# Performance work log

Measured on AMD Instinct MI355X. Metric: run time of the kernel, lower is better.

## Reference

```python
import jax, jax.numpy as jnp
import numpy as np

B, H, W, C = 2, 64, 64, 96
DIN, NST, RNK, K = 192, 16, 6, 4
L = H * W


def _make_ids():
    idx = np.arange(L).reshape(H, W)
    p0 = idx.reshape(-1)
    p1 = idx.T.reshape(-1)
    p2 = p0[::-1].copy()
    p3 = p1[::-1].copy()
    scan = np.stack([p0, p1, p2, p3]).astype(np.int32)
    inv = np.stack([np.argsort(p) for p in scan]).astype(np.int32)
    return jnp.asarray(scan), jnp.asarray(inv)


def setup_inputs() -> dict:
    key = jax.random.key(0)
    ks = jax.random.split(key, 10)
    scan_ids, inv_ids = _make_ids()
    std = RNK ** -0.5
    # dt bias init: inverse-softplus of dt ~ LogUniform(1e-3, 1e-1), as in VMM.dt_init
    u = jax.random.uniform(ks[5], (K, DIN))
    dt = jnp.exp(u * (np.log(0.1) - np.log(0.001)) + np.log(0.001))
    dt_b = dt + jnp.log(-jnp.expm1(-dt))
    return {
        "x": jax.random.normal(ks[0], (B, H, W, C), jnp.float32),
        "W_in": jax.random.normal(ks[1], (2 * DIN, C), jnp.float32) * 0.02,
        "conv_w": jax.random.normal(ks[2], (DIN, 1, 3, 3), jnp.float32) * 0.1,
        "conv_b": jnp.zeros((DIN,), jnp.float32),
        "x_proj_w": jax.random.normal(ks[3], (K, RNK + 2 * NST, DIN), jnp.float32) * 0.02,
        "dt_w": jax.random.uniform(ks[4], (K, DIN, RNK), jnp.float32, -std, std),
        "dt_b": dt_b.astype(jnp.float32),
        "A_logs": jnp.log(jnp.tile(jnp.arange(1, NST + 1, dtype=jnp.float32)[None], (K * DIN, 1))),
        "Ds": jnp.ones((K * DIN,), jnp.float32),
        "gate_w": jax.random.normal(ks[6], (4 * DIN, 4), jnp.float32) * 0.1,  # grouped 1x1 conv, groups=DIN
        "gate_b": jnp.zeros((4 * DIN,), jnp.float32),
        "ln_g": jnp.ones((DIN,), jnp.float32),
        "ln_b": jnp.zeros((DIN,), jnp.float32),
        "W_out": jax.random.normal(ks[7], (C, DIN), jnp.float32) * 0.02,
        "scan_ids": scan_ids,
        "inv_ids": inv_ids,
    }


def _forward(x, W_in, conv_w, conv_b, x_proj_w, dt_w, dt_b, A_logs, Ds, gate_w, gate_b, ln_g, ln_b, W_out, scan_ids, inv_ids):
    b, h, w, c = x.shape
    l = h * w
    din = conv_w.shape[0]
    k = x_proj_w.shape[0]
    nst = A_logs.shape[1]
    rnk = dt_w.shape[2]
    # in_proj + split into x / gate z
    xz = x @ W_in.T
    xc, z = jnp.split(xz, 2, axis=-1)
    xc = jnp.transpose(xc, (0, 3, 1, 2))  # (b, din, h, w)
    # depthwise 3x3 conv + SiLU
    xc = jax.lax.conv_general_dilated(
        xc, conv_w, (1, 1), "SAME", feature_group_count=din,
        dimension_numbers=("NCHW", "OIHW", "NCHW")) + conv_b[None, :, None, None]
    xc = jax.nn.silu(xc)
    # multi-directional gather (mair_ids_scan)
    xf = xc.reshape(b, din, l)
    xs = jnp.moveaxis(xf[:, :, scan_ids], 2, 1)  # (b, k, din, l)
    # x_proj (grouped 1x1 conv) -> dt, B, C
    x_dbl = jnp.einsum("bkdl,krd->bkrl", xs, x_proj_w)
    dts, Bs, Cs = jnp.split(x_dbl, [rnk, rnk + nst], axis=2)  # (b,k,rnk,l),(b,k,n,l),(b,k,n,l)
    delta = jax.nn.softplus(jnp.einsum("bkrl,kdr->bkdl", dts, dt_w) + dt_b[None, :, :, None])
    A = -jnp.exp(A_logs).reshape(k, din, nst)
    dA = jnp.exp(delta[..., None] * A[None, :, :, None, :])              # (b,k,d,l,n)
    dBu = (delta * xs)[..., None] * jnp.moveaxis(Bs, 2, 3)[:, :, None]   # (b,k,d,l,n)

    def step(hst, inp):
        da, dbu = inp
        hst = da * hst + dbu
        return hst, hst

    h0 = jnp.zeros((b, k, din, nst), jnp.float32)
    _, hs = jax.lax.scan(step, h0, (jnp.moveaxis(dA, 3, 0), jnp.moveaxis(dBu, 3, 0)))  # (l,b,k,d,n)
    ys = jnp.einsum("lbkdn,bknl->bkdl", hs, Cs) + xs * Ds.reshape(k, din)[None, :, :, None]
    # inverse scatter (mair_ids_inverse) + concat along channels
    y = jax.vmap(lambda yk, ik: yk[..., ik], in_axes=(1, 0), out_axes=1)(ys, inv_ids)
    y = y.reshape(b, k * din, h, w)
    # ShuffleAttn gating: group = din, group_channels = k
    shuf = y.reshape(b, k, din, h, w).transpose(0, 2, 1, 3, 4).reshape(b, k * din, h, w)
    pooled = shuf.mean(axis=(2, 3)).reshape(b, din, k)
    gate = jax.nn.sigmoid(jnp.einsum("bgi,goi->bgo", pooled, gate_w.reshape(din, k, k)) + gate_b.reshape(din, k))
    gate = gate.transpose(0, 2, 1).reshape(b, k * din)  # channel_rearrange
    y = y * gate[:, :, None, None]
    # sum the 4 direction branches
    y = y.reshape(b, k, din, h, w).sum(axis=1)
    y = jnp.transpose(y, (0, 2, 3, 1))  # (b,h,w,din)
    # LayerNorm(d_inner)
    mu = y.mean(-1, keepdims=True)
    var = ((y - mu) ** 2).mean(-1, keepdims=True)
    y = (y - mu) / jnp.sqrt(var + 1e-5) * ln_g + ln_b
    y = y * jax.nn.silu(z)
    return y @ W_out.T


def reference(x, W_in, conv_w, conv_b, x_proj_w, dt_w, dt_b, A_logs, Ds, gate_w, gate_b, ln_g, ln_b, W_out, scan_ids, inv_ids):
    return _forward(x, W_in, conv_w, conv_b, x_proj_w, dt_w, dt_b, A_logs, Ds, gate_w, gate_b, ln_g, ln_b, W_out, scan_ids, inv_ids)
```

## Files before the change

### kernel.cpp

```cpp
#include <hip/hip_runtime.h>
#include <math.h>

#define BB 2
#define CC 96
#define DIN 192
#define NST 16
#define RNK 6
#define KK 4
#define LL 4096
#define RTOT (RNK + 2*NST)


__global__ __launch_bounds__(256) void k_inproj(const float* __restrict__ x,
        const float* __restrict__ W_in, float* __restrict__ xc_pre,
        float* __restrict__ z_silu) {
    __shared__ float lx[96*65];
    __shared__ float wt[48*196];
    int b = blockIdx.y, z = blockIdx.z;
    int l0 = blockIdx.x * 64;
    int t = threadIdx.x;
    for (int i = 0; i < 24; ++i) {
        int e = t + 256*i;
        int l = e / 96, c = e % 96;
        lx[c*65 + l] = x[((size_t)(b*LL + l0 + l))*96 + c];
    }
    int lg = t & 15;
    int og = t >> 4;
    float acc[4][12];
    #pragma unroll
    for (int j = 0; j < 4; ++j)
        #pragma unroll
        for (int q = 0; q < 12; ++q) acc[j][q] = 0.f;
    for (int p = 0; p < 2; ++p) {
        __syncthreads();
        for (int i = 0; i < 36; ++i) {
            int e = t + 256*i;
            int cc = e % 48, oc = e / 48;
            wt[cc*196 + oc] = W_in[((size_t)(z*192 + oc))*96 + p*48 + cc];
        }
        __syncthreads();
        #pragma unroll 2
        for (int cc = 0; cc < 48; ++cc) {
            int c = p*48 + cc;
            float x0 = lx[c*65 + 4*lg + 0];
            float x1 = lx[c*65 + 4*lg + 1];
            float x2 = lx[c*65 + 4*lg + 2];
            float x3 = lx[c*65 + 4*lg + 3];
            const float* wr = &wt[cc*196 + 12*og];
            float4 w0 = *(const float4*)(wr);
            float4 w1 = *(const float4*)(wr + 4);
            float4 w2 = *(const float4*)(wr + 8);
            float wv[12] = {w0.x,w0.y,w0.z,w0.w, w1.x,w1.y,w1.z,w1.w,
                            w2.x,w2.y,w2.z,w2.w};
            #pragma unroll
            for (int q = 0; q < 12; ++q) {
                acc[0][q] += x0*wv[q];
                acc[1][q] += x1*wv[q];
                acc[2][q] += x2*wv[q];
                acc[3][q] += x3*wv[q];
            }
        }
    }
    float* dst = (z == 0) ? xc_pre : z_silu;
    #pragma unroll
    for (int j = 0; j < 4; ++j) {
        int l = l0 + 4*lg + j;
        size_t base = (size_t)(b*LL + l)*DIN + 12*og;
        #pragma unroll
        for (int q = 0; q < 12; ++q) {
            float v = acc[j][q];
            if (z) v = v / (1.f + __expf(-v));
            dst[base + q] = v;
        }
    }
}

__global__ __launch_bounds__(256) void k_conv(const float* __restrict__ xc,
        const float* __restrict__ cw, const float* __restrict__ cb,
        float* __restrict__ out) {
    int gid = blockIdx.x*256 + threadIdx.x;
    int d = gid % DIN;
    int r = gid / DIN;
    int l = r & 4095, b = r >> 12;
    int w = l & 63, h = l >> 6;
    float acc = cb[d];
    #pragma unroll
    for (int dh = -1; dh <= 1; ++dh) {
        int h2 = h + dh;
        bool okh = (h2 >= 0) && (h2 < 64);
        #pragma unroll
        for (int dw = -1; dw <= 1; ++dw) {
            int w2 = w + dw;
            if (okh && w2 >= 0 && w2 < 64)
                acc += xc[((size_t)(b*LL + h2*64 + w2))*DIN + d] * cw[d*9 + (dh+1)*3 + (dw+1)];
        }
    }
    out[((size_t)(b*LL + l))*DIN + d] = acc / (1.f + __expf(-acc));
}

__global__ __launch_bounds__(512) void k_proj(const float* __restrict__ xconv,
        const int* __restrict__ scan_ids, const float* __restrict__ xpw,
        float* __restrict__ dts, float* __restrict__ Bs, float* __restrict__ Cs) {
    __shared__ float lxs[96*65];
    __shared__ float lw[RTOT*96];
    __shared__ float lbc[64*33];
    __shared__ int lsid[64];
    int k = blockIdx.y, b = blockIdx.z;
    int l0 = blockIdx.x * 64;
    int t = threadIdx.x;
    if (t < 64) lsid[t] = scan_ids[k*LL + l0 + t];
    int l = t & 63;
    int rg = __builtin_amdgcn_readfirstlane(t >> 6);
    float acc[5];
    #pragma unroll
    for (int j = 0; j < 5; ++j) acc[j] = 0.f;
    for (int p = 0; p < 2; ++p) {
        __syncthreads();
        for (int i = 0; i < 12; ++i) {
            int e = t + 512*i;
            int dd = e % 96, ll = e / 96;
            lxs[dd*65 + ll] = xconv[((size_t)(b*LL + lsid[ll]))*DIN + p*96 + dd];
        }
        for (int i = 0; i < 8; ++i) {
            int e = t + 512*i;
            if (e < RTOT*96) {
                int r = e / 96, dd = e % 96;
                lw[r*96 + dd] = xpw[(size_t)k*RTOT*DIN + r*DIN + p*96 + dd];
            }
        }
        __syncthreads();
        for (int dd = 0; dd < 96; dd += 4) {
            float x0 = lxs[(dd+0)*65 + l];
            float x1 = lxs[(dd+1)*65 + l];
            float x2 = lxs[(dd+2)*65 + l];
            float x3 = lxs[(dd+3)*65 + l];
            #pragma unroll
            for (int j = 0; j < 5; ++j) {
                int r = rg + 8*j;
                if (r < RTOT) {
                    float4 w = *(const float4*)&lw[r*96 + dd];
                    acc[j] += x0*w.x + x1*w.y + x2*w.z + x3*w.w;
                }
            }
        }
    }
    int bk = b*KK + k;
    #pragma unroll
    for (int j = 0; j < 5; ++j) {
        int r = rg + 8*j;
        if (r < RNK)       dts[((size_t)bk*LL + l0 + l)*8 + r] = acc[j];
        else if (r < RTOT) lbc[l*33 + (r - RNK)] = acc[j];
    }
    __syncthreads();
    size_t rowb = ((size_t)bk*LL + l0)*NST;
    for (int i = 0; i < 2; ++i) {
        int e = t + 512*i;
        int n = e & 15, ll = e >> 4;
        Bs[rowb + ll*NST + n] = lbc[ll*33 + n];
        Cs[rowb + ll*NST + n] = lbc[ll*33 + 16 + n];
    }
}

__global__ __launch_bounds__(384) void k_scan1(const float* __restrict__ xconv,
        const float* __restrict__ Bs, const float* __restrict__ Cs,
        const float* __restrict__ dts, const float* __restrict__ dtw,
        const float* __restrict__ dtb,
        const int* __restrict__ scan_ids, const float* __restrict__ A_logs,
        const float* __restrict__ Ds,
        float* __restrict__ y_dirs, float* __restrict__ segA,
        float* __restrict__ segB, int SL) {
    int seg = blockIdx.x, bk = blockIdx.y;
    int b = bk >> 2, k = bk & 3;
    int t = threadIdx.x;
    int half = t & 1, d = t >> 1;
    int l0 = seg * SL;
    float Av[8];
    {
        const float4* ap = (const float4*)(A_logs + ((k*DIN + d)*NST + half*8));
        float4 a0 = ap[0], a1 = ap[1];
        Av[0]=-__expf(a0.x); Av[1]=-__expf(a0.y); Av[2]=-__expf(a0.z); Av[3]=-__expf(a0.w);
        Av[4]=-__expf(a1.x); Av[5]=-__expf(a1.y); Av[6]=-__expf(a1.z); Av[7]=-__expf(a1.w);
    }
    float Dv = Ds[k*DIN + d];
    float wdt[RNK];
    float bdt = dtb[k*DIN + d];
    #pragma unroll
    for (int r = 0; r < RNK; ++r) wdt[r] = dtw[(k*DIN + d)*RNK + r];
    float h[8];
    #pragma unroll
    for (int n = 0; n < 8; ++n) h[n] = 0.f;
    float sumdv = 0.f;
    const int* sid = scan_ids + k*LL + l0;
    int ln = sid[0];
    float xn = xconv[((size_t)(b*LL + ln))*DIN + d];
    for (int li = 0; li < SL; ++li) {
        int l = ln;
        float xv = xn;
        if (li + 1 < SL) {
            ln = sid[li + 1];
            xn = xconv[((size_t)(b*LL + ln))*DIN + d];
        }
        const float* dr = dts + ((size_t)bk*LL + l0 + li)*8;
        float aa = bdt;
        #pragma unroll
        for (int r = 0; r < RNK; ++r) aa += dr[r]*wdt[r];
        float dv = fmaxf(aa, 0.f) + __logf(1.f + __expf(-fabsf(aa)));
        sumdv += dv;
        float dxv = dv * xv;
        const float* br = Bs + ((size_t)bk*LL + l0 + li)*NST + half*8;
        const float* cr = Cs + ((size_t)bk*LL + l0 + li)*NST + half*8;
        float4 b0 = *(const float4*)br;
        float4 b1 = *(const float4*)(br + 4);
        float4 c0v = *(const float4*)cr;
        float4 c1v = *(const float4*)(cr + 4);
        float bb[8] = {b0.x,b0.y,b0.z,b0.w, b1.x,b1.y,b1.z,b1.w};
        float cc[8] = {c0v.x,c0v.y,c0v.z,c0v.w, c1v.x,c1v.y,c1v.z,c1v.w};
        float y = 0.f;
        #pragma unroll
        for (int n = 0; n < 8; ++n) {
            float e2 = __expf(dv * Av[n]);
            h[n] = e2*h[n] + dxv*bb[n];
            y += h[n]*cc[n];
        }
        y += __shfl_xor(y, 1);
        if (half == 0) {
            y += xv * Dv;
            y_dirs[((size_t)(bk*LL + l))*DIN + d] = y;
        }
    }
    float a[8];
    #pragma unroll
    for (int n = 0; n < 8; ++n) a[n] = __expf(Av[n]*sumdv);
    size_t base = (((size_t)bk*gridDim.x + seg)*DIN + d)*NST + half*8;
    *(float4*)&segA[base]     = make_float4(a[0],a[1],a[2],a[3]);
    *(float4*)&segA[base + 4] = make_float4(a[4],a[5],a[6],a[7]);
    *(float4*)&segB[base]     = make_float4(h[0],h[1],h[2],h[3]);
    *(float4*)&segB[base + 4] = make_float4(h[4],h[5],h[6],h[7]);
}

__global__ __launch_bounds__(256) void k_scan2(const float* segA,
        const float* segB, float* hinit, int SEGC) {
    int idx = blockIdx.x*256 + threadIdx.x;
    if (idx >= BB*KK*DIN*NST) return;
    int bk = idx / (DIN*NST);
    int dn = idx % (DIN*NST);
    const size_t stride = DIN*NST;
    size_t o = (size_t)bk*SEGC*stride + dn;
    float h = 0.f;
    for (int s = 0; s < SEGC; s += 8) {
        float av[8], bv[8];
        #pragma unroll
        for (int j = 0; j < 8; ++j) {
            av[j] = segA[o + j*stride];
            bv[j] = segB[o + j*stride];
        }
        #pragma unroll
        for (int j = 0; j < 8; ++j) {
            hinit[o + j*stride] = h;
            h = av[j]*h + bv[j];
        }
        o += 8*stride;
    }
}

__global__ __launch_bounds__(384) void k_apply(const float* __restrict__ Cs,
        const float* __restrict__ dts, const float* __restrict__ dtw,
        const float* __restrict__ dtb,
        const int* __restrict__ scan_ids, const float* __restrict__ A_logs,
        const float* __restrict__ hinit,
        float* __restrict__ y_dirs, float* __restrict__ poolsum, int SL) {
    int seg = blockIdx.x, bk = blockIdx.y;
    int b = bk >> 2, k = bk & 3;
    int t = threadIdx.x;
    int half = t & 1, d = t >> 1;
    int l0 = seg * SL;
    float Av[8];
    {
        const float4* ap = (const float4*)(A_logs + ((k*DIN + d)*NST + half*8));
        float4 a0 = ap[0], a1 = ap[1];
        Av[0]=-__expf(a0.x); Av[1]=-__expf(a0.y); Av[2]=-__expf(a0.z); Av[3]=-__expf(a0.w);
        Av[4]=-__expf(a1.x); Av[5]=-__expf(a1.y); Av[6]=-__expf(a1.z); Av[7]=-__expf(a1.w);
    }
    float Av0 = -__expf(A_logs[(k*DIN + d)*NST]);
    bool okl = true;
    #pragma unroll
    for (int q = 0; q < 8; ++q) {
        float m = (float)(half*8 + q + 1);
        okl = okl && (fabsf(Av[q] - m*Av0) <= 1e-4f*m);
    }
    int fast = __all(okl);
    float h0[8];
    {
        size_t base = (((size_t)bk*gridDim.x + seg)*DIN + d)*NST + half*8;
        float4 v0 = *(const float4*)&hinit[base];
        float4 v1 = *(const float4*)&hinit[base + 4];
        h0[0]=v0.x; h0[1]=v0.y; h0[2]=v0.z; h0[3]=v0.w;
        h0[4]=v1.x; h0[5]=v1.y; h0[6]=v1.z; h0[7]=v1.w;
    }
    float wdt[RNK];
    float bdt = dtb[k*DIN + d];
    #pragma unroll
    for (int r = 0; r < RNK; ++r) wdt[r] = dtw[(k*DIN + d)*RNK + r];
    float cum = 0.f;
    float pool = 0.f;
    const int* sid = scan_ids + k*LL + l0;
    for (int li = 0; li < SL; ++li) {
        int l = sid[li];
        const float* dr = dts + ((size_t)bk*LL + l0 + li)*8;
        float aa = bdt;
        #pragma unroll
        for (int r = 0; r < RNK; ++r) aa += dr[r]*wdt[r];
        cum += fmaxf(aa, 0.f) + __logf(1.f + __expf(-fabsf(aa)));
        const float* cr = Cs + ((size_t)bk*LL + l0 + li)*NST + half*8;
        float4 c0v = *(const float4*)cr;
        float4 c1v = *(const float4*)(cr + 4);
        float cc[8] = {c0v.x,c0v.y,c0v.z,c0v.w, c1v.x,c1v.y,c1v.z,c1v.w};
        float g;
        if (fast) {
            float E = __expf(Av0 * cum);
            g = 0.f;
            #pragma unroll
            for (int q = 7; q >= 0; --q) g = g*E + cc[q]*h0[q];
            g *= E;
            if (half) {
                float E2 = E*E, E4 = E2*E2;
                g *= E4*E4;
            }
        } else {
            g = 0.f;
            #pragma unroll
            for (int q = 0; q < 8; ++q)
                g += cc[q]*h0[q]*__expf(Av[q]*cum);
        }
        g += __shfl_xor(g, 1);
        if (half == 0) {
            size_t yo = ((size_t)(bk*LL + l))*DIN + d;
            float y = y_dirs[yo] + g;
            y_dirs[yo] = y;
            pool += y;
        }
    }
    if (half == 0) atomicAdd(&poolsum[(b*DIN + d)*KK + k], pool);
}

__global__ __launch_bounds__(256) void k_final(const float* __restrict__ y_dirs,
        const float* __restrict__ poolsum, const float* __restrict__ gw,
        const float* __restrict__ gb, const float* __restrict__ z_silu,
        const float* __restrict__ lng, const float* __restrict__ lnb,
        const float* __restrict__ Wout, float* __restrict__ out) {
    __shared__ float buf[16*193];
    __shared__ float lgate[DIN*KK];
    __shared__ float lmu[16], lrs[16];
    int b = blockIdx.y;
    int l0 = blockIdx.x * 16;
    int t = threadIdx.x;
    for (int e = t; e < DIN*KK; e += 256) {
        int d = e >> 2, o = e & 3;
        float acc = gb[d*KK + o];
        #pragma unroll
        for (int i = 0; i < KK; ++i)
            acc += (poolsum[(b*DIN + d)*KK + i] * (1.f/LL)) * gw[(d*KK + o)*KK + i];
        lgate[d*KK + o] = 1.f/(1.f + __expf(-acc));
    }
    __syncthreads();
    for (int i = 0; i < 12; ++i) {
        int e = t + 256*i;
        int d = e % DIN, l = e / DIN;
        float acc = 0.f;
        #pragma unroll
        for (int k = 0; k < KK; ++k)
            acc += y_dirs[((size_t)((b*KK + k)*LL + l0 + l))*DIN + d] * lgate[d*KK + k];
        buf[l*193 + d] = acc;
    }
    __syncthreads();
    int l2 = t >> 4, q = t & 15;
    float s = 0.f, s2 = 0.f;
    for (int i = 0; i < 12; ++i) {
        float v = buf[l2*193 + q + 16*i];
        s += v; s2 += v*v;
    }
    s += __shfl_xor(s, 1);  s2 += __shfl_xor(s2, 1);
    s += __shfl_xor(s, 2);  s2 += __shfl_xor(s2, 2);
    s += __shfl_xor(s, 4);  s2 += __shfl_xor(s2, 4);
    s += __shfl_xor(s, 8);  s2 += __shfl_xor(s2, 8);
    if (q == 0) {
        float mu = s * (1.f/DIN);
        float var = s2 * (1.f/DIN) - mu*mu;
        lmu[l2] = mu;
        lrs[l2] = rsqrtf(var + 1e-5f);
    }
    __syncthreads();
    for (int i = 0; i < 12; ++i) {
        int e = t + 256*i;
        int d = e % DIN, l = e / DIN;
        float v = buf[l*193 + d];
        float tv = (v - lmu[l]) * lrs[l] * lng[d] + lnb[d];
        tv *= z_silu[((size_t)(b*LL + l0 + l))*DIN + d];
        buf[l*193 + d] = tv;
    }
    __syncthreads();
    int l = t & 15;
    int c0 = (t >> 4) * 6;
    float acc[6];
    #pragma unroll
    for (int cc = 0; cc < 6; ++cc) acc[cc] = 0.f;
    for (int d = 0; d < DIN; ++d) {
        float v = buf[l*193 + d];
        #pragma unroll
        for (int cc = 0; cc < 6; ++cc)
            acc[cc] += v * Wout[(c0 + cc)*DIN + d];
    }
    #pragma unroll
    for (int cc = 0; cc < 6; ++cc)
        out[((size_t)(b*LL + l0 + l))*CC + c0 + cc] = acc[cc];
}

extern "C" void kernel_launch(void* const* d_in, const int* in_sizes, int n_in,
                              void* d_out, int out_size, void* d_ws, size_t ws_size,
                              hipStream_t stream) {
    const float* x      = (const float*)d_in[0];
    const float* W_in   = (const float*)d_in[1];
    const float* conv_w = (const float*)d_in[2];
    const float* conv_b = (const float*)d_in[3];
    const float* xpw    = (const float*)d_in[4];
    const float* dt_w   = (const float*)d_in[5];
    const float* dt_b   = (const float*)d_in[6];
    const float* A_logs = (const float*)d_in[7];
    const float* Ds     = (const float*)d_in[8];
    const float* gate_w = (const float*)d_in[9];
    const float* gate_b = (const float*)d_in[10];
    const float* ln_g   = (const float*)d_in[11];
    const float* ln_b   = (const float*)d_in[12];
    const float* W_out  = (const float*)d_in[13];
    const int* scan_ids = (const int*)d_in[14];
    float* out = (float*)d_out;

    const size_t baseF = 6291456ull + 2ull*1572864 + 262144ull + 2ull*524288 + 3072;
    int SEGC = 16;
    if ((baseF + 2ull*128*24576)*4 <= ws_size) SEGC = 128;
    else if ((baseF + 2ull*64*24576)*4 <= ws_size) SEGC = 64;
    else if ((baseF + 2ull*32*24576)*4 <= ws_size) SEGC = 32;
    int SL = LL / SEGC;
    size_t segF = (size_t)SEGC * 24576;

    float* ws      = (float*)d_ws;
    float* y_dirs  = ws;
    float* xc_pre  = ws;
    float* z_silu  = y_dirs  + 6291456;
    float* xconv   = z_silu  + 1572864;
    float* dts     = xconv   + 1572864;
    float* Bs      = dts     + 262144;
    float* Cs      = Bs      + 524288;
    float* poolsum = Cs      + 524288;
    float* segA    = poolsum + 3072;
    float* segB    = segA    + segF;
    float* hinit   = segA;

    hipMemsetAsync(poolsum, 0, 1536*sizeof(float), stream);

    k_inproj<<<dim3(LL/64, BB, 2), 256, 0, stream>>>(x, W_in, xc_pre, z_silu);
    k_conv<<<(BB*DIN*LL)/256, 256, 0, stream>>>(xc_pre, conv_w, conv_b, xconv);
    k_proj<<<dim3(LL/64, KK, BB), 512, 0, stream>>>(xconv, scan_ids, xpw,
                                                    dts, Bs, Cs);
    k_scan1<<<dim3(SEGC, BB*KK), 384, 0, stream>>>(xconv, Bs, Cs, dts, dt_w, dt_b,
                                                   scan_ids, A_logs, Ds,
                                                   y_dirs, segA, segB, SL);
    k_scan2<<<(BB*KK*DIN*NST + 255)/256, 256, 0, stream>>>(segA, segB, hinit, SEGC);
    k_apply<<<dim3(SEGC, BB*KK), 384, 0, stream>>>(Cs, dts, dt_w, dt_b,
                                                   scan_ids, A_logs, hinit,
                                                   y_dirs, poolsum, SL);
    k_final<<<dim3(LL/16, BB), 256, 0, stream>>>(y_dirs, poolsum, gate_w, gate_b,
                                                 z_silu, ln_g, ln_b, W_out, out);
}
```

Before: 280.4 us.

## Store per-step cumulative dt in scan1 and restructure apply and in-projection kernels

The first scan pass now writes the running sum of softplus(dt) for every step into a new workspace buffer. The apply kernel reads that sum instead of recomputing the dt projection and softplus, and each thread now handles all 16 states for alternating timesteps rather than splitting states across a lane pair with a shuffle. The in-projection kernel computes both x and z halves in one block, reusing the staged input tile, which halves the grid. Scan1 gets an unroll hint, and the minimum segment count rises to 32. This adds a large extra write and read of the cumulative-dt buffer and more registers per thread in apply.

```diff
diff --git a/kernel.cpp b/kernel.cpp
--- a/kernel.cpp
+++ b/kernel.cpp
@@ -16,7 +16,7 @@
         float* __restrict__ z_silu) {
     __shared__ float lx[96*65];
     __shared__ float wt[48*196];
-    int b = blockIdx.y, z = blockIdx.z;
+    int b = blockIdx.y;
     int l0 = blockIdx.x * 64;
     int t = threadIdx.x;
     for (int i = 0; i < 24; ++i) {
@@ -26,51 +26,53 @@
     }
     int lg = t & 15;
     int og = t >> 4;
-    float acc[4][12];
-    #pragma unroll
-    for (int j = 0; j < 4; ++j)
-        #pragma unroll
-        for (int q = 0; q < 12; ++q) acc[j][q] = 0.f;
-    for (int p = 0; p < 2; ++p) {
-        __syncthreads();
-        for (int i = 0; i < 36; ++i) {
-            int e = t + 256*i;
-            int cc = e % 48, oc = e / 48;
-            wt[cc*196 + oc] = W_in[((size_t)(z*192 + oc))*96 + p*48 + cc];
-        }
-        __syncthreads();
-        #pragma unroll 2
-        for (int cc = 0; cc < 48; ++cc) {
-            int c = p*48 + cc;
-            float x0 = lx[c*65 + 4*lg + 0];
-            float x1 = lx[c*65 + 4*lg + 1];
-            float x2 = lx[c*65 + 4*lg + 2];
-            float x3 = lx[c*65 + 4*lg + 3];
-            const float* wr = &wt[cc*196 + 12*og];
-            float4 w0 = *(const float4*)(wr);
-            float4 w1 = *(const float4*)(wr + 4);
-            float4 w2 = *(const float4*)(wr + 8);
-            float wv[12] = {w0.x,w0.y,w0.z,w0.w, w1.x,w1.y,w1.z,w1.w,
-                            w2.x,w2.y,w2.z,w2.w};
+    for (int z = 0; z < 2; ++z) {
+        float acc[4][12];
+        #pragma unroll
+        for (int j = 0; j < 4; ++j)
+            #pragma unroll
+            for (int q = 0; q < 12; ++q) acc[j][q] = 0.f;
+        for (int p = 0; p < 2; ++p) {
+            __syncthreads();
+            for (int i = 0; i < 36; ++i) {
+                int e = t + 256*i;
+                int cc = e % 48, oc = e / 48;
+                wt[cc*196 + oc] = W_in[((size_t)(z*192 + oc))*96 + p*48 + cc];
+            }
+            __syncthreads();
+            #pragma unroll 2
+            for (int cc = 0; cc < 48; ++cc) {
+                int c = p*48 + cc;
+                float x0 = lx[c*65 + 4*lg + 0];
+                float x1 = lx[c*65 + 4*lg + 1];
+                float x2 = lx[c*65 + 4*lg + 2];
+                float x3 = lx[c*65 + 4*lg + 3];
+                const float* wr = &wt[cc*196 + 12*og];
+                float4 w0 = *(const float4*)(wr);
+                float4 w1 = *(const float4*)(wr + 4);
+                float4 w2 = *(const float4*)(wr + 8);
+                float wv[12] = {w0.x,w0.y,w0.z,w0.w, w1.x,w1.y,w1.z,w1.w,
+                                w2.x,w2.y,w2.z,w2.w};
+                #pragma unroll
+                for (int q = 0; q < 12; ++q) {
+                    acc[0][q] += x0*wv[q];
+                    acc[1][q] += x1*wv[q];
+                    acc[2][q] += x2*wv[q];
+                    acc[3][q] += x3*wv[q];
+                }
+            }
+        }
+        float* dst = (z == 0) ? xc_pre : z_silu;
+        #pragma unroll
+        for (int j = 0; j < 4; ++j) {
+            int l = l0 + 4*lg + j;
+            size_t base = (size_t)(b*LL + l)*DIN + 12*og;
             #pragma unroll
             for (int q = 0; q < 12; ++q) {
-                acc[0][q] += x0*wv[q];
-                acc[1][q] += x1*wv[q];
-                acc[2][q] += x2*wv[q];
-                acc[3][q] += x3*wv[q];
+                float v = acc[j][q];
+                if (z) v = v / (1.f + __expf(-v));
+                dst[base + q] = v;
             }
-        }
-    }
-    float* dst = (z == 0) ? xc_pre : z_silu;
-    #pragma unroll
-    for (int j = 0; j < 4; ++j) {
-        int l = l0 + 4*lg + j;
-        size_t base = (size_t)(b*LL + l)*DIN + 12*og;
-        #pragma unroll
-        for (int q = 0; q < 12; ++q) {
-            float v = acc[j][q];
-            if (z) v = v / (1.f + __expf(-v));
-            dst[base + q] = v;
         }
     }
 }
@@ -167,8 +169,8 @@
         const float* __restrict__ dtb,
         const int* __restrict__ scan_ids, const float* __restrict__ A_logs,
         const float* __restrict__ Ds,
-        float* __restrict__ y_dirs, float* __restrict__ segA,
-        float* __restrict__ segB, int SL) {
+        float* __restrict__ y_dirs, float* __restrict__ cumseg,
+        float* __restrict__ segA, float* __restrict__ segB, int SL) {
     int seg = blockIdx.x, bk = blockIdx.y;
     int b = bk >> 2, k = bk & 3;
     int t = threadIdx.x;
@@ -193,6 +195,7 @@
     const int* sid = scan_ids + k*LL + l0;
     int ln = sid[0];
     float xn = xconv[((size_t)(b*LL + ln))*DIN + d];
+    #pragma unroll 4
     for (int li = 0; li < SL; ++li) {
         int l = ln;
         float xv = xn;
@@ -226,6 +229,7 @@
         if (half == 0) {
             y += xv * Dv;
             y_dirs[((size_t)(bk*LL + l))*DIN + d] = y;
+            cumseg[((size_t)bk*LL + l0 + li)*DIN + d] = sumdv;
         }
     }
     float a[8];
@@ -264,83 +268,76 @@
 }
 
 __global__ __launch_bounds__(384) void k_apply(const float* __restrict__ Cs,
-        const float* __restrict__ dts, const float* __restrict__ dtw,
-        const float* __restrict__ dtb,
+        const float* __restrict__ cumseg,
         const int* __restrict__ scan_ids, const float* __restrict__ A_logs,
         const float* __restrict__ hinit,
         float* __restrict__ y_dirs, float* __restrict__ poolsum, int SL) {
     int seg = blockIdx.x, bk = blockIdx.y;
     int b = bk >> 2, k = bk & 3;
     int t = threadIdx.x;
-    int half = t & 1, d = t >> 1;
+    int half = (t >= 192) ? 1 : 0;
+    int d = t - half*192;
     int l0 = seg * SL;
-    float Av[8];
+    float Av[16];
     {
-        const float4* ap = (const float4*)(A_logs + ((k*DIN + d)*NST + half*8));
-        float4 a0 = ap[0], a1 = ap[1];
-        Av[0]=-__expf(a0.x); Av[1]=-__expf(a0.y); Av[2]=-__expf(a0.z); Av[3]=-__expf(a0.w);
-        Av[4]=-__expf(a1.x); Av[5]=-__expf(a1.y); Av[6]=-__expf(a1.z); Av[7]=-__expf(a1.w);
-    }
-    float Av0 = -__expf(A_logs[(k*DIN + d)*NST]);
+        const float4* ap = (const float4*)(A_logs + (k*DIN + d)*NST);
+        #pragma unroll
+        for (int q = 0; q < 4; ++q) {
+            float4 v = ap[q];
+            Av[4*q+0] = -__expf(v.x); Av[4*q+1] = -__expf(v.y);
+            Av[4*q+2] = -__expf(v.z); Av[4*q+3] = -__expf(v.w);
+        }
+    }
+    float Av0 = Av[0];
     bool okl = true;
     #pragma unroll
-    for (int q = 0; q < 8; ++q) {
-        float m = (float)(half*8 + q + 1);
+    for (int q = 0; q < 16; ++q) {
+        float m = (float)(q + 1);
         okl = okl && (fabsf(Av[q] - m*Av0) <= 1e-4f*m);
     }
     int fast = __all(okl);
-    float h0[8];
+    float h0[16];
     {
-        size_t base = (((size_t)bk*gridDim.x + seg)*DIN + d)*NST + half*8;
-        float4 v0 = *(const float4*)&hinit[base];
-        float4 v1 = *(const float4*)&hinit[base + 4];
-        h0[0]=v0.x; h0[1]=v0.y; h0[2]=v0.z; h0[3]=v0.w;
-        h0[4]=v1.x; h0[5]=v1.y; h0[6]=v1.z; h0[7]=v1.w;
-    }
-    float wdt[RNK];
-    float bdt = dtb[k*DIN + d];
-    #pragma unroll
-    for (int r = 0; r < RNK; ++r) wdt[r] = dtw[(k*DIN + d)*RNK + r];
-    float cum = 0.f;
+        const float4* hp = (const float4*)(hinit +
+            (((size_t)bk*gridDim.x + seg)*DIN + d)*NST);
+        #pragma unroll
+        for (int q = 0; q < 4; ++q) {
+            float4 v = hp[q];
+            h0[4*q+0] = v.x; h0[4*q+1] = v.y; h0[4*q+2] = v.z; h0[4*q+3] = v.w;
+        }
+    }
+    const int* sid = scan_ids + k*LL + l0;
     float pool = 0.f;
-    const int* sid = scan_ids + k*LL + l0;
-    for (int li = 0; li < SL; ++li) {
+    for (int i = 0; i < SL; i += 2) {
+        int li = i + half;
+        float cum = cumseg[((size_t)bk*LL + l0 + li)*DIN + d];
         int l = sid[li];
-        const float* dr = dts + ((size_t)bk*LL + l0 + li)*8;
-        float aa = bdt;
-        #pragma unroll
-        for (int r = 0; r < RNK; ++r) aa += dr[r]*wdt[r];
-        cum += fmaxf(aa, 0.f) + __logf(1.f + __expf(-fabsf(aa)));
-        const float* cr = Cs + ((size_t)bk*LL + l0 + li)*NST + half*8;
-        float4 c0v = *(const float4*)cr;
-        float4 c1v = *(const float4*)(cr + 4);
-        float cc[8] = {c0v.x,c0v.y,c0v.z,c0v.w, c1v.x,c1v.y,c1v.z,c1v.w};
+        const float* cr = Cs + ((size_t)bk*LL + l0 + li)*NST;
+        float cc[16];
+        #pragma unroll
+        for (int q = 0; q < 4; ++q) {
+            float4 v = *(const float4*)(cr + 4*q);
+            cc[4*q+0] = v.x; cc[4*q+1] = v.y; cc[4*q+2] = v.z; cc[4*q+3] = v.w;
+        }
         float g;
         if (fast) {
             float E = __expf(Av0 * cum);
             g = 0.f;
             #pragma unroll
-            for (int q = 7; q >= 0; --q) g = g*E + cc[q]*h0[q];
+            for (int q = 15; q >= 0; --q) g = g*E + cc[q]*h0[q];
             g *= E;
-            if (half) {
-                float E2 = E*E, E4 = E2*E2;
-                g *= E4*E4;
-            }
         } else {
             g = 0.f;
             #pragma unroll
-            for (int q = 0; q < 8; ++q)
+            for (int q = 0; q < 16; ++q)
                 g += cc[q]*h0[q]*__expf(Av[q]*cum);
         }
-        g += __shfl_xor(g, 1);
-        if (half == 0) {
-            size_t yo = ((size_t)(bk*LL + l))*DIN + d;
-            float y = y_dirs[yo] + g;
-            y_dirs[yo] = y;
-            pool += y;
-        }
-    }
-    if (half == 0) atomicAdd(&poolsum[(b*DIN + d)*KK + k], pool);
+        size_t yo = ((size_t)(bk*LL + l))*DIN + d;
+        float y = y_dirs[yo] + g;
+        y_dirs[yo] = y;
+        pool += y;
+    }
+    atomicAdd(&poolsum[(b*DIN + d)*KK + k], pool);
 }
 
 __global__ __launch_bounds__(256) void k_final(const float* __restrict__ y_dirs,
@@ -435,11 +432,11 @@
     const int* scan_ids = (const int*)d_in[14];
     float* out = (float*)d_out;
 
-    const size_t baseF = 6291456ull + 2ull*1572864 + 262144ull + 2ull*524288 + 3072;
-    int SEGC = 16;
+    const size_t baseF = 6291456ull + 2ull*1572864 + 262144ull + 2ull*524288
+                       + 3072 + 6291456ull;
+    int SEGC = 32;
     if ((baseF + 2ull*128*24576)*4 <= ws_size) SEGC = 128;
     else if ((baseF + 2ull*64*24576)*4 <= ws_size) SEGC = 64;
-    else if ((baseF + 2ull*32*24576)*4 <= ws_size) SEGC = 32;
     int SL = LL / SEGC;
     size_t segF = (size_t)SEGC * 24576;
 
@@ -452,21 +449,22 @@
     float* Bs      = dts     + 262144;
     float* Cs      = Bs      + 524288;
     float* poolsum = Cs      + 524288;
-    float* segA    = poolsum + 3072;
+    float* cumseg  = poolsum + 3072;
+    float* segA    = cumseg  + 6291456;
     float* segB    = segA    + segF;
     float* hinit   = segA;
 
     hipMemsetAsync(poolsum, 0, 1536*sizeof(float), stream);
 
-    k_inproj<<<dim3(LL/64, BB, 2), 256, 0, stream>>>(x, W_in, xc_pre, z_silu);
+    k_inproj<<<dim3(LL/64, BB), 256, 0, stream>>>(x, W_in, xc_pre, z_silu);
     k_conv<<<(BB*DIN*LL)/256, 256, 0, stream>>>(xc_pre, conv_w, conv_b, xconv);
     k_proj<<<dim3(LL/64, KK, BB), 512, 0, stream>>>(xconv, scan_ids, xpw,
                                                     dts, Bs, Cs);
     k_scan1<<<dim3(SEGC, BB*KK), 384, 0, stream>>>(xconv, Bs, Cs, dts, dt_w, dt_b,
                                                    scan_ids, A_logs, Ds,
-                                                   y_dirs, segA, segB, SL);
+                                                   y_dirs, cumseg, segA, segB, SL);
     k_scan2<<<(BB*KK*DIN*NST + 255)/256, 256, 0, stream>>>(segA, segB, hinit, SEGC);
-    k_apply<<<dim3(SEGC, BB*KK), 384, 0, stream>>>(Cs, dts, dt_w, dt_b,
+    k_apply<<<dim3(SEGC, BB*KK), 384, 0, stream>>>(Cs, cumseg,
                                                    scan_ids, A_logs, hinit,
                                                    y_dirs, poolsum, SL);
     k_final<<<dim3(LL/16, BB), 256, 0, stream>>>(y_dirs, poolsum, gate_w, gate_b,
```

New measurement: 297.2 us. +6.0%, slower.
